# Kernel optimization log

Hardware: AMD Instinct MI355X
Metric: run time of the kernel (lower is better)

## Reference

```python
import jax, jax.numpy as jnp
import numpy as np

IN_DIM, HID_DIM, OUT_DIM = 768, 512, 256
B = 1024


def setup_inputs() -> dict:
    key = jax.random.key(0)
    ks = jax.random.split(key, 8)
    s = lambda fan_in: 1.0 / np.sqrt(fan_in)
    return {
        "combin_emb": jax.random.normal(ks[0], (B, IN_DIM), jnp.float32),
        "s_emb": jax.random.normal(ks[1], (B, HID_DIM), jnp.float32),
        # fn1: Linear(hid, hid); torch weight layout [out, in]
        "W1": jax.random.uniform(ks[2], (HID_DIM, HID_DIM), jnp.float32, -s(HID_DIM), s(HID_DIM)),
        "b1": jax.random.uniform(ks[3], (HID_DIM,), jnp.float32, -s(HID_DIM), s(HID_DIM)),
        # fn2: Linear(in, hid)
        "W2": jax.random.uniform(ks[4], (HID_DIM, IN_DIM), jnp.float32, -s(IN_DIM), s(IN_DIM)),
        "b2": jax.random.uniform(ks[5], (HID_DIM,), jnp.float32, -s(IN_DIM), s(IN_DIM)),
        # fn3: Linear(hid, out)
        "W3": jax.random.uniform(ks[6], (OUT_DIM, HID_DIM), jnp.float32, -s(HID_DIM), s(HID_DIM)),
        "b3": jax.random.uniform(ks[7], (OUT_DIM,), jnp.float32, -s(HID_DIM), s(HID_DIM)),
    }


def reference(combin_emb, s_emb, W1, b1, W2, b2, W3, b3):
    scale = 1.0 / np.sqrt(HID_DIM)
    c_emb = combin_emb @ W2.T + b2          # [B, H] query
    t_emb = s_emb @ W1.T + b1               # [B, H] key
    # outer-product scores: [B, H, H], softmax over key axis (last)
    scores = scale * c_emb[:, :, None] * t_emb[:, None, :]
    attn = jax.nn.softmax(scores, axis=-1)
    # value is raw s_emb: [B, H, H] @ [B, H] -> [B, H]
    out = jax.nn.relu(jnp.einsum('bij,bj->bi', attn, s_emb))
    return out @ W3.T + b3                  # [B, OUT]
```

## Files before the change

### kernel.cpp

```cpp
#include <hip/hip_runtime.h>
#include <hip/hip_bf16.h>


#define B_SZ 1024
#define HID 512
#define IN_D 768
#define OUT_D 256
#define NK 8

typedef float floatx16 __attribute__((ext_vector_type(16)));
typedef short short8  __attribute__((ext_vector_type(8)));

__device__ __forceinline__ unsigned pack_bf16(float a, float b) {
    unsigned ua = __float_as_uint(a) + 0x8000u;
    unsigned ub = __float_as_uint(b) + 0x8000u;
    return __builtin_amdgcn_perm(ub, ua, 0x07060302);
}
__device__ __forceinline__ uint4 pack8(float4 lo, float4 hi) {
    uint4 v;
    v.x = pack_bf16(lo.x, lo.y); v.y = pack_bf16(lo.z, lo.w);
    v.z = pack_bf16(hi.x, hi.y); v.w = pack_bf16(hi.z, hi.w);
    return v;
}

template<bool A_BF16>
__device__ __forceinline__ void gemm32_direct(
    const void* Aip, const float* __restrict__ Wp,
    const float* __restrict__ bias, float* __restrict__ C,
    int N, int K, int nch, int row0, int col0,
    float (*__restrict__ redf)[64])
{
    const int tid  = threadIdx.x;
    const int w    = tid >> 6;
    const int lane = tid & 63;
    const int m    = lane & 31;
    const int kh   = lane >> 5;
    const int k0   = w * nch * 16 + kh * 8;

    const float* pw = Wp + (size_t)(col0 + m) * K + k0;
    float4 b0 = *(const float4*)pw, b1 = *(const float4*)(pw + 4);

    floatx16 acc = {};

    if (A_BF16) {
        const __hip_bfloat16* pa =
            (const __hip_bfloat16*)Aip + (size_t)(row0 + m) * K + k0;
        uint4 av = *(const uint4*)pa;
        for (int c = 0; c < nch; ++c) {
            uint4 af = av;
            uint4 bf = pack8(b0, b1);
            if (c + 1 < nch) {
                pa += 16; pw += 16;
                av = *(const uint4*)pa;
                b0 = *(const float4*)pw; b1 = *(const float4*)(pw + 4);
            }
            acc = __builtin_amdgcn_mfma_f32_32x32x16_bf16(
                *(short8*)&af, *(short8*)&bf, acc, 0, 0, 0);
        }
    } else {
        const float* pa = (const float*)Aip + (size_t)(row0 + m) * K + k0;
        float4 a0 = *(const float4*)pa, a1 = *(const float4*)(pa + 4);
        for (int c = 0; c < nch; ++c) {
            uint4 af = pack8(a0, a1);
            uint4 bf = pack8(b0, b1);
            if (c + 1 < nch) {
                pa += 16; pw += 16;
                a0 = *(const float4*)pa; a1 = *(const float4*)(pa + 4);
                b0 = *(const float4*)pw; b1 = *(const float4*)(pw + 4);
            }
            acc = __builtin_amdgcn_mfma_f32_32x32x16_bf16(
                *(short8*)&af, *(short8*)&bf, acc, 0, 0, 0);
        }
    }

    #pragma unroll
    for (int q = 0; q < 16; ++q) redf[w * 16 + q][lane] = acc[q];
    __syncthreads();

    const int ccol = col0 + m;
    const float bv = bias[ccol];
    float* cb = C + (size_t)(row0 + 8 * w + 4 * kh) * N + ccol;
    #pragma unroll
    for (int i = 0; i < 4; ++i) {
        const int q = 4 * w + i;
        float s = redf[q][lane] + redf[16 + q][lane]
                + redf[32 + q][lane] + redf[48 + q][lane];
        cb[(size_t)i * N] = s + bv;
    }
}

__global__ __launch_bounds__(256) void gemm_ct_k(
    const float* __restrict__ combin, const float* __restrict__ W2,
    const float* __restrict__ b2, float* __restrict__ c_emb,
    const float* __restrict__ s_emb, const float* __restrict__ W1,
    const float* __restrict__ b1, float* __restrict__ t_emb)
{
    __shared__ float redf[64][64];
    int id = blockIdx.x;
    if (id < 512) {
        gemm32_direct<false>(combin, W2, b2, c_emb, HID, IN_D, 12,
                             (id >> 4) * 32, (id & 15) * 32, redf);
    } else {
        id -= 512;
        gemm32_direct<false>(s_emb, W1, b1, t_emb, HID, HID, 8,
                             (id >> 4) * 32, (id & 15) * 32, redf);
    }
}

__global__ __launch_bounds__(256) void gemm_out_k(
    const __hip_bfloat16* __restrict__ o2, const float* __restrict__ W3,
    const float* __restrict__ b3, float* __restrict__ out)
{
    __shared__ float redf[64][64];
    int id = blockIdx.x;
    gemm32_direct<true>(o2, W3, b3, out, OUT_D, HID, 8,
                        (id >> 3) * 32, (id & 7) * 32, redf);
}

__global__ __launch_bounds__(256) void attn_taylor(
    const float* __restrict__ c_emb, const float* __restrict__ t_emb,
    const float* __restrict__ s_emb, unsigned* __restrict__ o2u)
{
    __shared__ float t_s[HID];
    __shared__ float v_s[HID];
    __shared__ float part[256][17];
    __shared__ float red2[16][16];
    __shared__ float fin[16];

    const int b = blockIdx.x, tid = threadIdx.x;

    if (tid < 128) ((float4*)t_s)[tid] = ((const float4*)(t_emb + (size_t)b * HID))[tid];
    else           ((float4*)v_s)[tid - 128] = ((const float4*)(s_emb + (size_t)b * HID))[tid - 128];
    float2 cc = ((const float2*)(c_emb + (size_t)b * HID))[tid];
    __syncthreads();

    float2 tt = ((float2*)t_s)[tid];
    float2 vv = ((float2*)v_s)[tid];
    float tp0 = 1.f, tp1 = 1.f;
    #pragma unroll
    for (int k = 0; k < NK; ++k) {
        part[tid][k]      = tp0 + tp1;
        part[tid][k + NK] = fmaf(tp0, vv.x, tp1 * vv.y);
        tp0 *= tt.x; tp1 *= tt.y;
    }
    __syncthreads();
    {
        int k = tid & 15, g = tid >> 4;
        float s = 0.f;
        #pragma unroll
        for (int r = 0; r < 16; ++r) s += part[g * 16 + r][k];
        red2[g][k] = s;
    }
    __syncthreads();
    if (tid < 16) {
        float s = 0.f;
        #pragma unroll
        for (int g = 0; g < 16; ++g) s += red2[g][tid];
        fin[tid] = s;
    }
    __syncthreads();

    const float invf[NK] = {1.f, 1.f, 0.5f, 1.f / 6.f, 1.f / 24.f,
                            1.f / 120.f, 1.f / 720.f, 1.f / 5040.f};
    float cp[NK], cm[NK];
    #pragma unroll
    for (int k = 0; k < NK; ++k) {
        cp[k] = fin[k] * invf[k];
        cm[k] = fin[k + NK] * invf[k];
    }

    const float scale = 0.04419417382415922f;
    float a0 = scale * cc.x, a1 = scale * cc.y;
    float n0 = cm[NK - 1], d0 = cp[NK - 1], n1 = cm[NK - 1], d1 = cp[NK - 1];
    #pragma unroll
    for (int k = NK - 2; k >= 0; --k) {
        n0 = fmaf(n0, a0, cm[k]); d0 = fmaf(d0, a0, cp[k]);
        n1 = fmaf(n1, a1, cm[k]); d1 = fmaf(d1, a1, cp[k]);
    }
    float r0 = n0 * __builtin_amdgcn_rcpf(d0);
    float r1 = n1 * __builtin_amdgcn_rcpf(d1);
    r0 = r0 > 0.f ? r0 : 0.f;
    r1 = r1 > 0.f ? r1 : 0.f;
    o2u[(size_t)b * (HID / 2) + tid] = pack_bf16(r0, r1);
}

extern "C" void kernel_launch(void* const* d_in, const int* in_sizes, int n_in,
                              void* d_out, int out_size, void* d_ws, size_t ws_size,
                              hipStream_t stream)
{
    const float* combin = (const float*)d_in[0];
    const float* s_emb  = (const float*)d_in[1];
    const float* W1     = (const float*)d_in[2];
    const float* b1     = (const float*)d_in[3];
    const float* W2     = (const float*)d_in[4];
    const float* b2     = (const float*)d_in[5];
    const float* W3     = (const float*)d_in[6];
    const float* b3     = (const float*)d_in[7];
    float* out = (float*)d_out;

    float* ws = (float*)d_ws;
    float* c_emb = ws;
    float* t_emb = ws + (size_t)B_SZ * HID;
    unsigned* o2u = (unsigned*)(ws + (size_t)2 * B_SZ * HID);

    gemm_ct_k<<<1024, 256, 0, stream>>>(combin, W2, b2, c_emb, s_emb, W1, b1, t_emb);
    attn_taylor<<<B_SZ, 256, 0, stream>>>(c_emb, t_emb, s_emb, o2u);
    gemm_out_k<<<256, 256, 0, stream>>>((const __hip_bfloat16*)o2u, W3, b3, out);
}
```

Baseline: 98.32 us.

## Fuse three kernels into one cooperative persistent kernel with grid syncs

Merges the two input GEMMs, the Taylor-series attention and the output GEMM into a single cooperative kernel. It uses grid-wide syncs between stages and 512-thread blocks that each process two jobs at once. The attention reduction now uses wave shuffles instead of shared-memory partial sums, and the output GEMM splits K across 8 waves. The aim is to remove the launch overhead and gaps between kernels, at the cost of grid.sync latency and a grid capped by occupancy.

Result: slower. 173.2 us (+76.1%).

```diff
diff --git a/kernel.cpp b/kernel.cpp
--- a/kernel.cpp
+++ b/kernel.cpp
@@ -1,5 +1,8 @@
 #include <hip/hip_runtime.h>
 #include <hip/hip_bf16.h>
+#include <hip/hip_cooperative_groups.h>
+
+namespace cg = cooperative_groups;
 
 
 #define B_SZ 1024
@@ -23,63 +26,60 @@
     return v;
 }
 
-template<bool A_BF16>
-__device__ __forceinline__ void gemm32_direct(
-    const void* Aip, const float* __restrict__ Wp,
-    const float* __restrict__ bias, float* __restrict__ C,
-    int N, int K, int nch, int row0, int col0,
-    float (*__restrict__ redf)[64])
-{
-    const int tid  = threadIdx.x;
-    const int w    = tid >> 6;
-    const int lane = tid & 63;
-    const int m    = lane & 31;
-    const int kh   = lane >> 5;
-    const int k0   = w * nch * 16 + kh * 8;
-
-    const float* pw = Wp + (size_t)(col0 + m) * K + k0;
+template<int NCH>
+__device__ __forceinline__ floatx16 kloop_f32(
+    const float* __restrict__ pa, const float* __restrict__ pw)
+{
+    float4 a0 = *(const float4*)pa, a1 = *(const float4*)(pa + 4);
     float4 b0 = *(const float4*)pw, b1 = *(const float4*)(pw + 4);
-
     floatx16 acc = {};
-
-    if (A_BF16) {
-        const __hip_bfloat16* pa =
-            (const __hip_bfloat16*)Aip + (size_t)(row0 + m) * K + k0;
-        uint4 av = *(const uint4*)pa;
-        for (int c = 0; c < nch; ++c) {
-            uint4 af = av;
-            uint4 bf = pack8(b0, b1);
-            if (c + 1 < nch) {
-                pa += 16; pw += 16;
-                av = *(const uint4*)pa;
-                b0 = *(const float4*)pw; b1 = *(const float4*)(pw + 4);
-            }
-            acc = __builtin_amdgcn_mfma_f32_32x32x16_bf16(
-                *(short8*)&af, *(short8*)&bf, acc, 0, 0, 0);
-        }
-    } else {
-        const float* pa = (const float*)Aip + (size_t)(row0 + m) * K + k0;
-        float4 a0 = *(const float4*)pa, a1 = *(const float4*)(pa + 4);
-        for (int c = 0; c < nch; ++c) {
-            uint4 af = pack8(a0, a1);
-            uint4 bf = pack8(b0, b1);
-            if (c + 1 < nch) {
-                pa += 16; pw += 16;
-                a0 = *(const float4*)pa; a1 = *(const float4*)(pa + 4);
-                b0 = *(const float4*)pw; b1 = *(const float4*)(pw + 4);
-            }
-            acc = __builtin_amdgcn_mfma_f32_32x32x16_bf16(
-                *(short8*)&af, *(short8*)&bf, acc, 0, 0, 0);
-        }
-    }
-
+    #pragma unroll
+    for (int c = 0; c < NCH; ++c) {
+        uint4 af = pack8(a0, a1);
+        uint4 bf = pack8(b0, b1);
+        if (c + 1 < NCH) {
+            pa += 16; pw += 16;
+            a0 = *(const float4*)pa; a1 = *(const float4*)(pa + 4);
+            b0 = *(const float4*)pw; b1 = *(const float4*)(pw + 4);
+        }
+        acc = __builtin_amdgcn_mfma_f32_32x32x16_bf16(
+            *(short8*)&af, *(short8*)&bf, acc, 0, 0, 0);
+    }
+    return acc;
+}
+
+template<int NCH>
+__device__ __forceinline__ floatx16 kloop_bf16(
+    const __hip_bfloat16* __restrict__ pa, const float* __restrict__ pw)
+{
+    uint4 av = *(const uint4*)pa;
+    float4 b0 = *(const float4*)pw, b1 = *(const float4*)(pw + 4);
+    floatx16 acc = {};
+    #pragma unroll
+    for (int c = 0; c < NCH; ++c) {
+        uint4 af = av;
+        uint4 bf = pack8(b0, b1);
+        if (c + 1 < NCH) {
+            pa += 16; pw += 16;
+            av = *(const uint4*)pa;
+            b0 = *(const float4*)pw; b1 = *(const float4*)(pw + 4);
+        }
+        acc = __builtin_amdgcn_mfma_f32_32x32x16_bf16(
+            *(short8*)&af, *(short8*)&bf, acc, 0, 0, 0);
+    }
+    return acc;
+}
+
+__device__ __forceinline__ void reduce_store(
+    const floatx16& acc, float (*__restrict__ redf)[64],
+    const float* __restrict__ bias, float* __restrict__ C, int N,
+    int row0, int col0, int w, int lane, int m, int kh)
+{
     #pragma unroll
     for (int q = 0; q < 16; ++q) redf[w * 16 + q][lane] = acc[q];
     __syncthreads();
-
-    const int ccol = col0 + m;
-    const float bv = bias[ccol];
-    float* cb = C + (size_t)(row0 + 8 * w + 4 * kh) * N + ccol;
+    const float bv = bias[col0 + m];
+    float* cb = C + (size_t)(row0 + 8 * w + 4 * kh) * N + col0 + m;
     #pragma unroll
     for (int i = 0; i < 4; ++i) {
         const int q = 4 * w + i;
@@ -87,101 +87,128 @@
                 + redf[32 + q][lane] + redf[48 + q][lane];
         cb[(size_t)i * N] = s + bv;
     }
-}
-
-__global__ __launch_bounds__(256) void gemm_ct_k(
-    const float* __restrict__ combin, const float* __restrict__ W2,
-    const float* __restrict__ b2, float* __restrict__ c_emb,
-    const float* __restrict__ s_emb, const float* __restrict__ W1,
-    const float* __restrict__ b1, float* __restrict__ t_emb)
-{
-    __shared__ float redf[64][64];
-    int id = blockIdx.x;
-    if (id < 512) {
-        gemm32_direct<false>(combin, W2, b2, c_emb, HID, IN_D, 12,
-                             (id >> 4) * 32, (id & 15) * 32, redf);
-    } else {
-        id -= 512;
-        gemm32_direct<false>(s_emb, W1, b1, t_emb, HID, HID, 8,
-                             (id >> 4) * 32, (id & 15) * 32, redf);
-    }
-}
-
-__global__ __launch_bounds__(256) void gemm_out_k(
-    const __hip_bfloat16* __restrict__ o2, const float* __restrict__ W3,
-    const float* __restrict__ b3, float* __restrict__ out)
-{
-    __shared__ float redf[64][64];
-    int id = blockIdx.x;
-    gemm32_direct<true>(o2, W3, b3, out, OUT_D, HID, 8,
-                        (id >> 3) * 32, (id & 7) * 32, redf);
-}
-
-__global__ __launch_bounds__(256) void attn_taylor(
-    const float* __restrict__ c_emb, const float* __restrict__ t_emb,
-    const float* __restrict__ s_emb, unsigned* __restrict__ o2u)
-{
-    __shared__ float t_s[HID];
-    __shared__ float v_s[HID];
-    __shared__ float part[256][17];
-    __shared__ float red2[16][16];
-    __shared__ float fin[16];
-
-    const int b = blockIdx.x, tid = threadIdx.x;
-
-    if (tid < 128) ((float4*)t_s)[tid] = ((const float4*)(t_emb + (size_t)b * HID))[tid];
-    else           ((float4*)v_s)[tid - 128] = ((const float4*)(s_emb + (size_t)b * HID))[tid - 128];
-    float2 cc = ((const float2*)(c_emb + (size_t)b * HID))[tid];
     __syncthreads();
-
-    float2 tt = ((float2*)t_s)[tid];
-    float2 vv = ((float2*)v_s)[tid];
-    float tp0 = 1.f, tp1 = 1.f;
-    #pragma unroll
-    for (int k = 0; k < NK; ++k) {
-        part[tid][k]      = tp0 + tp1;
-        part[tid][k + NK] = fmaf(tp0, vv.x, tp1 * vv.y);
-        tp0 *= tt.x; tp1 *= tt.y;
-    }
-    __syncthreads();
-    {
-        int k = tid & 15, g = tid >> 4;
-        float s = 0.f;
-        #pragma unroll
-        for (int r = 0; r < 16; ++r) s += part[g * 16 + r][k];
-        red2[g][k] = s;
-    }
-    __syncthreads();
-    if (tid < 16) {
-        float s = 0.f;
-        #pragma unroll
-        for (int g = 0; g < 16; ++g) s += red2[g][tid];
-        fin[tid] = s;
-    }
-    __syncthreads();
-
-    const float invf[NK] = {1.f, 1.f, 0.5f, 1.f / 6.f, 1.f / 24.f,
-                            1.f / 120.f, 1.f / 720.f, 1.f / 5040.f};
-    float cp[NK], cm[NK];
-    #pragma unroll
-    for (int k = 0; k < NK; ++k) {
-        cp[k] = fin[k] * invf[k];
-        cm[k] = fin[k + NK] * invf[k];
-    }
-
-    const float scale = 0.04419417382415922f;
-    float a0 = scale * cc.x, a1 = scale * cc.y;
-    float n0 = cm[NK - 1], d0 = cp[NK - 1], n1 = cm[NK - 1], d1 = cp[NK - 1];
-    #pragma unroll
-    for (int k = NK - 2; k >= 0; --k) {
-        n0 = fmaf(n0, a0, cm[k]); d0 = fmaf(d0, a0, cp[k]);
-        n1 = fmaf(n1, a1, cm[k]); d1 = fmaf(d1, a1, cp[k]);
-    }
-    float r0 = n0 * __builtin_amdgcn_rcpf(d0);
-    float r1 = n1 * __builtin_amdgcn_rcpf(d1);
-    r0 = r0 > 0.f ? r0 : 0.f;
-    r1 = r1 > 0.f ? r1 : 0.f;
-    o2u[(size_t)b * (HID / 2) + tid] = pack_bf16(r0, r1);
+}
+
+__global__ __launch_bounds__(512, 4) void fused_all(
+    const float* __restrict__ combin, const float* __restrict__ s_emb,
+    const float* __restrict__ W1, const float* __restrict__ b1,
+    const float* __restrict__ W2, const float* __restrict__ b2,
+    const float* __restrict__ W3, const float* __restrict__ b3,
+    float* __restrict__ c_emb, float* __restrict__ t_emb,
+    unsigned* __restrict__ o2u, float* __restrict__ out)
+{
+    __shared__ float redf[2][64][64];
+    __shared__ float redp[2][4][2 * NK];
+
+    cg::grid_group grid = cg::this_grid();
+
+    const int tid  = threadIdx.x;
+    const int h    = tid >> 8;
+    const int t2   = tid & 255;
+    const int w4   = t2 >> 6;
+    const int lane = tid & 63;
+    const int m    = lane & 31;
+    const int kh   = lane >> 5;
+    const int nb2  = gridDim.x * 2;
+
+    for (int job = blockIdx.x * 2 + h; job < 1024; job += nb2) {
+        if (job < 512) {
+            const int row0 = (job >> 4) * 32, col0 = (job & 15) * 32;
+            const int k0 = w4 * 12 * 16 + kh * 8;
+            floatx16 acc = kloop_f32<12>(
+                combin + (size_t)(row0 + m) * IN_D + k0,
+                W2     + (size_t)(col0 + m) * IN_D + k0);
+            reduce_store(acc, redf[h], b2, c_emb, HID, row0, col0, w4, lane, m, kh);
+        } else {
+            const int j = job - 512;
+            const int row0 = (j >> 4) * 32, col0 = (j & 15) * 32;
+            const int k0 = w4 * 8 * 16 + kh * 8;
+            floatx16 acc = kloop_f32<8>(
+                s_emb + (size_t)(row0 + m) * HID + k0,
+                W1    + (size_t)(col0 + m) * HID + k0);
+            reduce_store(acc, redf[h], b1, t_emb, HID, row0, col0, w4, lane, m, kh);
+        }
+    }
+    grid.sync();
+
+    for (int b = blockIdx.x * 2 + h; b < B_SZ; b += nb2) {
+        const float2 tt = *(const float2*)(t_emb + (size_t)b * HID + 2 * t2);
+        const float2 vv = *(const float2*)(s_emb + (size_t)b * HID + 2 * t2);
+        const float2 cc = *(const float2*)(c_emb + (size_t)b * HID + 2 * t2);
+
+        float val[2 * NK];
+        float tp0 = 1.f, tp1 = 1.f;
+        #pragma unroll
+        for (int k = 0; k < NK; ++k) {
+            val[k]      = tp0 + tp1;
+            val[NK + k] = fmaf(tp0, vv.x, tp1 * vv.y);
+            tp0 *= tt.x; tp1 *= tt.y;
+        }
+        #pragma unroll
+        for (int off = 1; off < 64; off <<= 1)
+            #pragma unroll
+            for (int k = 0; k < 2 * NK; ++k)
+                val[k] += __shfl_xor(val[k], off);
+        if (lane == 0)
+            #pragma unroll
+            for (int k = 0; k < 2 * NK; ++k) redp[h][w4][k] = val[k];
+        __syncthreads();
+
+        const float invf[NK] = {1.f, 1.f, 0.5f, 1.f / 6.f, 1.f / 24.f,
+                                1.f / 120.f, 1.f / 720.f, 1.f / 5040.f};
+        float cp[NK], cm[NK];
+        #pragma unroll
+        for (int k = 0; k < NK; ++k) {
+            cp[k] = (redp[h][0][k] + redp[h][1][k]
+                   + redp[h][2][k] + redp[h][3][k]) * invf[k];
+            cm[k] = (redp[h][0][NK + k] + redp[h][1][NK + k]
+                   + redp[h][2][NK + k] + redp[h][3][NK + k]) * invf[k];
+        }
+
+        const float scale = 0.04419417382415922f;
+        const float a0 = scale * cc.x, a1 = scale * cc.y;
+        float n0 = cm[NK - 1], d0 = cp[NK - 1];
+        float n1 = cm[NK - 1], d1 = cp[NK - 1];
+        #pragma unroll
+        for (int k = NK - 2; k >= 0; --k) {
+            n0 = fmaf(n0, a0, cm[k]); d0 = fmaf(d0, a0, cp[k]);
+            n1 = fmaf(n1, a1, cm[k]); d1 = fmaf(d1, a1, cp[k]);
+        }
+        float r0v = n0 * __builtin_amdgcn_rcpf(d0);
+        float r1v = n1 * __builtin_amdgcn_rcpf(d1);
+        r0v = r0v > 0.f ? r0v : 0.f;
+        r1v = r1v > 0.f ? r1v : 0.f;
+        o2u[(size_t)b * (HID / 2) + t2] = pack_bf16(r0v, r1v);
+        __syncthreads();
+    }
+    grid.sync();
+
+    for (int tile = blockIdx.x; tile < 256; tile += gridDim.x) {
+        const int w8 = tid >> 6;
+        const int row0 = (tile >> 3) * 32, col0 = (tile & 7) * 32;
+        const int k0 = w8 * 64 + kh * 8;
+        floatx16 acc = kloop_bf16<4>(
+            (const __hip_bfloat16*)o2u + (size_t)(row0 + m) * HID + k0,
+            W3 + (size_t)(col0 + m) * HID + k0);
+
+        float* rf = &redf[0][0][0];
+        #pragma unroll
+        for (int q = 0; q < 16; ++q) rf[(w8 * 16 + q) * 64 + lane] = acc[q];
+        __syncthreads();
+
+        const float bv = b3[col0 + m];
+        #pragma unroll
+        for (int i = 0; i < 2; ++i) {
+            const int q = 2 * w8 + i;
+            float s = 0.f;
+            #pragma unroll
+            for (int ww = 0; ww < 8; ++ww) s += rf[(ww * 16 + q) * 64 + lane];
+            const int rr = (q & 3) + 8 * (q >> 2) + 4 * kh;
+            out[(size_t)(row0 + rr) * OUT_D + col0 + m] = s + bv;
+        }
+        __syncthreads();
+    }
 }
 
 extern "C" void kernel_launch(void* const* d_in, const int* in_sizes, int n_in,
@@ -199,11 +226,28 @@
     float* out = (float*)d_out;
 
     float* ws = (float*)d_ws;
-    float* c_emb = ws;
-    float* t_emb = ws + (size_t)B_SZ * HID;
-    unsigned* o2u = (unsigned*)(ws + (size_t)2 * B_SZ * HID);
-
-    gemm_ct_k<<<1024, 256, 0, stream>>>(combin, W2, b2, c_emb, s_emb, W1, b1, t_emb);
-    attn_taylor<<<B_SZ, 256, 0, stream>>>(c_emb, t_emb, s_emb, o2u);
-    gemm_out_k<<<256, 256, 0, stream>>>((const __hip_bfloat16*)o2u, W3, b3, out);
-}
+    float*    c_emb = ws;
+    float*    t_emb = ws + (size_t)B_SZ * HID;
+    unsigned* o2u   = (unsigned*)(ws + (size_t)2 * B_SZ * HID);
+
+    static int nblk = 0;
+    if (nblk == 0) {
+        int occ = 0, cu = 256;
+        hipOccupancyMaxActiveBlocksPerMultiprocessor(
+            &occ, (const void*)fused_all, 512, 0);
+        hipDeviceProp_t prop;
+        if (hipGetDeviceProperties(&prop, 0) == hipSuccess &&
+            prop.multiProcessorCount > 0)
+            cu = prop.multiProcessorCount;
+        if (occ < 1) occ = 1;
+        long cap = (long)occ * cu;
+        nblk = cap > 512 ? 512 : (int)cap;
+        if (nblk < 1) nblk = 1;
+    }
+
+    void* args[] = {(void*)&combin, (void*)&s_emb, (void*)&W1, (void*)&b1,
+                    (void*)&W2, (void*)&b2, (void*)&W3, (void*)&b3,
+                    (void*)&c_emb, (void*)&t_emb, (void*)&o2u, (void*)&out};
+    hipLaunchCooperativeKernel((const void*)fused_all, dim3(nblk), dim3(512),
+                               args, 0, stream);
+}
```
